# Performance work log

Hardware: AMD Instinct MI355X
Metric: run time of the kernel (lower is better)

## Reference

```python
import jax, jax.numpy as jnp
import numpy as np

B, NX, NQ, NU = 32768, 512, 128, 64
STD = 0.02


def setup_inputs() -> dict:
    key = jax.random.key(0)
    ks = jax.random.split(key, 8)
    p = lambda k, sh: jax.random.normal(k, sh, dtype=jnp.float32) * STD
    xi = jax.random.normal(ks[0], (B, NX), dtype=jnp.float32)
    u = jax.random.normal(ks[1], (B, NU), dtype=jnp.float32)
    A = p(ks[2], (NX, NX))
    B1 = p(ks[3], (NX, NQ))
    B2 = p(ks[4], (NX, NU))
    C1 = p(ks[5], (NQ, NX))
    # D11 from updateParameters is strictly lower triangular (inv(Lambda) @ tril(H4,-1)),
    # which is what makes the forward substitution loop well-posed.
    D11 = jnp.tril(p(ks[6], (NQ, NQ)), -1)
    D12 = p(ks[7], (NQ, NU))
    # bias=False in __init__ -> zero biases (non-trainable in torch, harmless here)
    bx = jnp.zeros((NX,), dtype=jnp.float32)
    bv = jnp.zeros((NQ,), dtype=jnp.float32)
    return dict(xi=xi, u=u, A=A, B1=B1, B2=B2, C1=C1, D11=D11, D12=D12, bx=bx, bv=bv)


def reference(xi, u, A, B1, B2, C1, D11, D12, bx, bv):
    # Hoist the parts of v_i that do not depend on w out of the recurrence:
    # v_i = xi @ C1[i] + u @ D12[i] + bv[i] + w @ D11[i]
    base = xi @ C1.T + u @ D12.T + bv          # [B, nq]
    nq = D11.shape[0]
    w0 = jnp.zeros_like(base)                   # [B, nq]

    # Sequential forward substitution over the nq nonlinear states.
    # Unset entries of w are zero, exactly matching the torch loop (D11 is
    # strictly lower triangular so only already-computed entries contribute).
    def step(w, xs):
        i, d_row, b_col = xs                    # d_row: [nq], b_col: [B]
        v = b_col + w @ d_row                   # [B]
        return w.at[:, i].set(jnp.tanh(v)), None

    w, _ = jax.lax.scan(step, w0, (jnp.arange(nq), D11, base.T))

    # xi_{+} = A xi + B1 w + B2 u + bx
    return xi @ A.T + w @ B1.T + u @ B2.T + bx
```

## Files before the change

kernel.cpp:

```cpp
#include <hip/hip_runtime.h>
#include <hip/hip_bf16.h>

#define BSZ 32768
#define NXD 512
#define NQD 128
#define NUD 64

typedef __attribute__((ext_vector_type(8))) unsigned short u16x8;
typedef __attribute__((ext_vector_type(8))) __bf16 bf16x8;
typedef __attribute__((ext_vector_type(4))) float f32x4;

#define DEVINL static __device__ __forceinline__

DEVINL unsigned short f2bf(float x) {
  __bf16 h = (__bf16)x;
  return __builtin_bit_cast(unsigned short, h);
}

DEVINL void gload_lds16(const ushort* g, ushort* l) {
  __builtin_amdgcn_global_load_lds(
      (const __attribute__((address_space(1))) void*)g,
      (__attribute__((address_space(3))) void*)l, 16, 0, 0);
}

DEVINL bf16x8 ld_frag(const ushort* p) {
  return __builtin_bit_cast(bf16x8, *(const u16x8*)p);
}

DEVINL float tanh_fast(float x) {
  float e2 = __builtin_amdgcn_exp2f(x * 2.88539008f);
  float r = __builtin_amdgcn_rcpf(e2 + 1.f);
  return __builtin_fmaf(-2.f, r, 1.f);
}

DEVINL void cvt8(const float* src, ushort* dst, int i) {
  const float4* s = (const float4*)src;
  float4 a = s[i * 2], b = s[i * 2 + 1];
  u16x8 v;
  v[0] = f2bf(a.x); v[1] = f2bf(a.y); v[2] = f2bf(a.z); v[3] = f2bf(a.w);
  v[4] = f2bf(b.x); v[5] = f2bf(b.y); v[6] = f2bf(b.z); v[7] = f2bf(b.w);
  *(u16x8*)(dst + (size_t)i * 8) = v;
}

__global__ __launch_bounds__(256) void prep(
    const float* __restrict__ xi, const float* __restrict__ u,
    const float* __restrict__ A, const float* __restrict__ B1,
    const float* __restrict__ B2, const float* __restrict__ C1,
    const float* __restrict__ D11, const float* __restrict__ D12,
    ushort* __restrict__ xib, ushort* __restrict__ ub,
    ushort* __restrict__ Wv, ushort* __restrict__ Wo,
    float* __restrict__ Dt) {
  int idx = blockIdx.x * 256 + threadIdx.x;
  const int N0 = BSZ * NXD / 8;
  const int N1 = N0 + BSZ * NUD / 8;
  const int N2 = N1 + NQD * (NXD + NUD);
  const int N3 = N2 + NXD * 704;
  const int N4 = N3 + NQD * NQD;
  if (idx < N0) {
    cvt8(xi, xib, idx);
  } else if (idx < N1) {
    cvt8(u, ub, idx - N0);
  } else if (idx < N2) {
    int f = idx - N1;
    int i = f / (NXD + NUD);
    int k = f - i * (NXD + NUD);
    Wv[f] = f2bf(k < NXD ? C1[i * NXD + k] : D12[i * NUD + (k - NXD)]);
  } else if (idx < N3) {
    int f = idx - N2;
    int n = f / 704;
    int k = f - n * 704;
    float v;
    if (k < NXD)            v = A[n * NXD + k];
    else if (k < NXD + NQD) v = B1[n * NQD + (k - NXD)];
    else                    v = B2[n * NUD + (k - NXD - NQD)];
    Wo[f] = f2bf(v);
  } else if (idx < N4) {
    int f = idx - N3;
    int j = f >> 7, i = f & (NQD - 1);
    Dt[f] = D11[i * NQD + j];
  }
}

template <int BM, int BN, int WM, int WN>
__global__ __launch_bounds__(WM* WN * 64, 2) void gemm2ph(
    const ushort* __restrict__ p0, int e0, int ld0,
    const ushort* __restrict__ p1, int e1, int ld1,
    const ushort* __restrict__ p2, int ld2,
    const ushort* __restrict__ W, int K,
    const float* __restrict__ biasN,
    float* __restrict__ out, int ldo) {
  constexpr int THREADS = WM * WN * 64;
  constexpr int BK = 64;
  constexpr int MREP = BM / WM / 16;
  constexpr int NREP = BN / WN / 16;
  constexpr int PASSA = BM * 8 / THREADS;
  constexpr int PASSB = BN * 8 / THREADS;

  __shared__ ushort ldsA[2][BM * BK];
  __shared__ ushort ldsB[2][BN * BK];

  const int tid = threadIdx.x;
  const int lane = tid & 63;
  const int wv = tid >> 6;
  const int wm = wv / WN, wn = wv % WN;
  const int rowBase = blockIdx.x * BM;
  const int colBase = blockIdx.y * BN;

  f32x4 acc[MREP][NREP];
#pragma unroll
  for (int m = 0; m < MREP; ++m)
#pragma unroll
    for (int n = 0; n < NREP; ++n) acc[m][n] = (f32x4){0.f, 0.f, 0.f, 0.f};

  const int NT = K / BK;

  auto stage = [&](int b, int kt) {
    const int k0 = kt * BK;
    const ushort* src; int kk, ld;
    if (k0 < e0)      { src = p0; kk = k0;      ld = ld0; }
    else if (k0 < e1) { src = p1; kk = k0 - e0; ld = ld1; }
    else              { src = p2; kk = k0 - e1; ld = ld2; }
#pragma unroll
    for (int p = 0; p < PASSA; ++p) {
      int idx = p * THREADS + tid;
      int row = idx >> 3, slot = idx & 7;
      int gcol = kk + ((slot ^ (row & 7)) << 3);
      gload_lds16(src + (size_t)(rowBase + row) * ld + gcol,
                  &ldsA[b][idx * 8]);
    }
#pragma unroll
    for (int p = 0; p < PASSB; ++p) {
      int idx = p * THREADS + tid;
      int row = idx >> 3, slot = idx & 7;
      int gcol = k0 + ((slot ^ (row & 7)) << 3);
      gload_lds16(W + (size_t)(colBase + row) * K + gcol, &ldsB[b][idx * 8]);
    }
  };

  stage(0, 0);
  __syncthreads();

  int cur = 0;
  for (int kt = 0; kt < NT; ++kt) {
    if (kt + 1 < NT) stage(cur ^ 1, kt + 1);

#pragma unroll
    for (int ks = 0; ks < 2; ++ks) {
      bf16x8 af[MREP], bfr[NREP];
#pragma unroll
      for (int m = 0; m < MREP; ++m) {
        int r = wm * (BM / WM) + m * 16 + (lane & 15);
        int slot = (ks * 4 + (lane >> 4)) ^ (r & 7);
        af[m] = ld_frag(&ldsA[cur][r * BK + slot * 8]);
      }
#pragma unroll
      for (int n = 0; n < NREP; ++n) {
        int r = wn * (BN / WN) + n * 16 + (lane & 15);
        int slot = (ks * 4 + (lane >> 4)) ^ (r & 7);
        bfr[n] = ld_frag(&ldsB[cur][r * BK + slot * 8]);
      }
#pragma unroll
      for (int m = 0; m < MREP; ++m)
#pragma unroll
        for (int n = 0; n < NREP; ++n)
          acc[m][n] = __builtin_amdgcn_mfma_f32_16x16x32_bf16(
              af[m], bfr[n], acc[m][n], 0, 0, 0);
    }
    __syncthreads();
    cur ^= 1;
  }

  const int cl = lane & 15;
  const int rq = (lane >> 4) * 4;
#pragma unroll
  for (int m = 0; m < MREP; ++m) {
    int row = rowBase + wm * (BM / WM) + m * 16 + rq;
#pragma unroll
    for (int n = 0; n < NREP; ++n) {
      int col = colBase + wn * (BN / WN) + n * 16 + cl;
      float bn = biasN[col];
      float* o = out + (size_t)row * ldo + col;
#pragma unroll
      for (int j = 0; j < 4; ++j) o[(size_t)j * ldo] = acc[m][n][j] + bn;
    }
  }
}

__global__ __launch_bounds__(512) void recur8(const float* __restrict__ base,
                                              const float* __restrict__ Dt,
                                              ushort* __restrict__ wout) {
  __shared__ float ldsD[NQD * NQD];
  const int tid = threadIdx.x;
  for (int c = tid; c < NQD * NQD / 4; c += 512)
    ((float4*)ldsD)[c] = ((const float4*)Dt)[c];
  __syncthreads();

  const int lane = tid & 63;
  const int wid = tid >> 6;
  const int s = lane & 7;
  const int grp = lane >> 3;
  const int row = blockIdx.x * 64 + wid * 8 + grp;
  const int laneBase = lane & 56;

  float4 acc[4];
  {
    const float4* bp4 = (const float4*)(base + (size_t)row * NQD);
#pragma unroll
    for (int k = 0; k < 4; ++k) acc[k] = bp4[s + 8 * k];
  }

  const float4* D4 = (const float4*)ldsD;

#pragma unroll
  for (int j = 0; j < NQD; ++j) {
    const int src = (j >> 2) & 7;
    const int r = j >> 5;
    const int e = j & 3;
    float tv = tanh_fast(acc[r][e]);
    float wj = __shfl(tv, laneBase | src, 64);
    if (s == src) acc[r][e] = wj;
#pragma unroll
    for (int k = 0; k < 4; ++k) {
      if (j < 32 * k + 32) {
        float4 d = D4[j * 32 + s + 8 * k];
        acc[k].x += d.x * wj; acc[k].y += d.y * wj;
        acc[k].z += d.z * wj; acc[k].w += d.w * wj;
      }
    }
  }

  ushort* orow = wout + (size_t)row * NQD;
#pragma unroll
  for (int k = 0; k < 4; ++k) {
    ushort4 v;
    v.x = f2bf(acc[k].x); v.y = f2bf(acc[k].y);
    v.z = f2bf(acc[k].z); v.w = f2bf(acc[k].w);
    *(ushort4*)(orow + 4 * (s + 8 * k)) = v;
  }
}

extern "C" void kernel_launch(void* const* d_in, const int* in_sizes, int n_in,
                              void* d_out, int out_size, void* d_ws, size_t ws_size,
                              hipStream_t stream) {
  const float* xi  = (const float*)d_in[0];
  const float* u   = (const float*)d_in[1];
  const float* A   = (const float*)d_in[2];
  const float* B1  = (const float*)d_in[3];
  const float* B2  = (const float*)d_in[4];
  const float* C1  = (const float*)d_in[5];
  const float* D11 = (const float*)d_in[6];
  const float* D12 = (const float*)d_in[7];
  const float* bx  = (const float*)d_in[8];
  const float* bv  = (const float*)d_in[9];
  float* out = (float*)d_out;

  char* ws = (char*)d_ws;
  ushort* xib  = (ushort*)(ws + 0);
  ushort* ub   = (ushort*)(ws + 33554432);
  ushort* wb   = (ushort*)(ws + 37748736);
  float*  base = (float*)(ws + 46137344);
  ushort* Wv   = (ushort*)(ws + 62914560);
  ushort* Wo   = (ushort*)(ws + 63062016);
  float*  Dt   = (float*)(ws + 63782912);

  {
    int total = BSZ * NXD / 8 + BSZ * NUD / 8 + NQD * (NXD + NUD) + NXD * 704 +
                NQD * NQD;
    prep<<<dim3((total + 255) / 256), 256, 0, stream>>>(
        xi, u, A, B1, B2, C1, D11, D12, xib, ub, Wv, Wo, Dt);
  }

  gemm2ph<128, 128, 2, 2><<<dim3(BSZ / 128, 1), 256, 0, stream>>>(
      xib, NXD, NXD, ub, NXD + NUD, NUD, ub, NUD, Wv, NXD + NUD, bv, base, NQD);

  recur8<<<dim3(BSZ / 64), 512, 0, stream>>>(base, Dt, wb);

  gemm2ph<256, 256, 2, 4><<<dim3(BSZ / 256, NXD / 256), 512, 0, stream>>>(
      xib, NXD, NXD, wb, NXD + NQD, NQD, ub, NUD, Wo, NXD + NQD + NUD, bx, out,
      NXD);
}
```

Measured before the change: 211.9 us.

## Replace double-buffered GEMM with single-buffer 128x128 tiles at higher occupancy

Result: faster. 205.7 us (-2.9%).

```diff
diff --git a/kernel.cpp b/kernel.cpp
--- a/kernel.cpp
+++ b/kernel.cpp
@@ -81,28 +81,28 @@
   }
 }
 
-template <int BM, int BN, int WM, int WN>
-__global__ __launch_bounds__(WM* WN * 64, 2) void gemm2ph(
+template <int BM, int BN>
+__global__ __launch_bounds__(256, 4) void gemm97(
     const ushort* __restrict__ p0, int e0, int ld0,
     const ushort* __restrict__ p1, int e1, int ld1,
     const ushort* __restrict__ p2, int ld2,
     const ushort* __restrict__ W, int K,
     const float* __restrict__ biasN,
     float* __restrict__ out, int ldo) {
-  constexpr int THREADS = WM * WN * 64;
+  constexpr int THREADS = 256;
   constexpr int BK = 64;
-  constexpr int MREP = BM / WM / 16;
-  constexpr int NREP = BN / WN / 16;
+  constexpr int MREP = BM / 2 / 16;
+  constexpr int NREP = BN / 2 / 16;
   constexpr int PASSA = BM * 8 / THREADS;
   constexpr int PASSB = BN * 8 / THREADS;
 
-  __shared__ ushort ldsA[2][BM * BK];
-  __shared__ ushort ldsB[2][BN * BK];
+  __shared__ ushort ldsA[BM * BK];
+  __shared__ ushort ldsB[BN * BK];
 
   const int tid = threadIdx.x;
   const int lane = tid & 63;
   const int wv = tid >> 6;
-  const int wm = wv / WN, wn = wv % WN;
+  const int wm = wv >> 1, wn = wv & 1;
   const int rowBase = blockIdx.x * BM;
   const int colBase = blockIdx.y * BN;
 
@@ -114,50 +114,43 @@
 
   const int NT = K / BK;
 
-  auto stage = [&](int b, int kt) {
+  for (int kt = 0; kt < NT; ++kt) {
     const int k0 = kt * BK;
     const ushort* src; int kk, ld;
     if (k0 < e0)      { src = p0; kk = k0;      ld = ld0; }
     else if (k0 < e1) { src = p1; kk = k0 - e0; ld = ld1; }
     else              { src = p2; kk = k0 - e1; ld = ld2; }
+
 #pragma unroll
     for (int p = 0; p < PASSA; ++p) {
       int idx = p * THREADS + tid;
       int row = idx >> 3, slot = idx & 7;
       int gcol = kk + ((slot ^ (row & 7)) << 3);
-      gload_lds16(src + (size_t)(rowBase + row) * ld + gcol,
-                  &ldsA[b][idx * 8]);
+      gload_lds16(src + (size_t)(rowBase + row) * ld + gcol, &ldsA[idx * 8]);
     }
 #pragma unroll
     for (int p = 0; p < PASSB; ++p) {
       int idx = p * THREADS + tid;
       int row = idx >> 3, slot = idx & 7;
       int gcol = k0 + ((slot ^ (row & 7)) << 3);
-      gload_lds16(W + (size_t)(colBase + row) * K + gcol, &ldsB[b][idx * 8]);
-    }
-  };
-
-  stage(0, 0);
-  __syncthreads();
-
-  int cur = 0;
-  for (int kt = 0; kt < NT; ++kt) {
-    if (kt + 1 < NT) stage(cur ^ 1, kt + 1);
+      gload_lds16(W + (size_t)(colBase + row) * K + gcol, &ldsB[idx * 8]);
+    }
+    __syncthreads();
 
 #pragma unroll
     for (int ks = 0; ks < 2; ++ks) {
       bf16x8 af[MREP], bfr[NREP];
 #pragma unroll
       for (int m = 0; m < MREP; ++m) {
-        int r = wm * (BM / WM) + m * 16 + (lane & 15);
+        int r = wm * (BM / 2) + m * 16 + (lane & 15);
         int slot = (ks * 4 + (lane >> 4)) ^ (r & 7);
-        af[m] = ld_frag(&ldsA[cur][r * BK + slot * 8]);
+        af[m] = ld_frag(&ldsA[r * BK + slot * 8]);
       }
 #pragma unroll
       for (int n = 0; n < NREP; ++n) {
-        int r = wn * (BN / WN) + n * 16 + (lane & 15);
+        int r = wn * (BN / 2) + n * 16 + (lane & 15);
         int slot = (ks * 4 + (lane >> 4)) ^ (r & 7);
-        bfr[n] = ld_frag(&ldsB[cur][r * BK + slot * 8]);
+        bfr[n] = ld_frag(&ldsB[r * BK + slot * 8]);
       }
 #pragma unroll
       for (int m = 0; m < MREP; ++m)
@@ -167,17 +160,16 @@
               af[m], bfr[n], acc[m][n], 0, 0, 0);
     }
     __syncthreads();
-    cur ^= 1;
   }
 
   const int cl = lane & 15;
   const int rq = (lane >> 4) * 4;
 #pragma unroll
   for (int m = 0; m < MREP; ++m) {
-    int row = rowBase + wm * (BM / WM) + m * 16 + rq;
+    int row = rowBase + wm * (BM / 2) + m * 16 + rq;
 #pragma unroll
     for (int n = 0; n < NREP; ++n) {
-      int col = colBase + wn * (BN / WN) + n * 16 + cl;
+      int col = colBase + wn * (BN / 2) + n * 16 + cl;
       float bn = biasN[col];
       float* o = out + (size_t)row * ldo + col;
 #pragma unroll
@@ -270,12 +262,12 @@
         xi, u, A, B1, B2, C1, D11, D12, xib, ub, Wv, Wo, Dt);
   }
 
-  gemm2ph<128, 128, 2, 2><<<dim3(BSZ / 128, 1), 256, 0, stream>>>(
+  gemm97<128, 128><<<dim3(BSZ / 128, 1), 256, 0, stream>>>(
       xib, NXD, NXD, ub, NXD + NUD, NUD, ub, NUD, Wv, NXD + NUD, bv, base, NQD);
 
   recur8<<<dim3(BSZ / 64), 512, 0, stream>>>(base, Dt, wb);
 
-  gemm2ph<256, 256, 2, 4><<<dim3(BSZ / 256, NXD / 256), 512, 0, stream>>>(
+  gemm97<128, 128><<<dim3(BSZ / 128, NXD / 128), 256, 0, stream>>>(
       xib, NXD, NXD, wb, NXD + NQD, NQD, ub, NUD, Wo, NXD + NQD + NUD, bx, out,
       NXD);
 }
```
